# Optimization experiments

Measured on AMD Instinct MI355X. Metric: run time of the kernel, lower is better.

The kernel has to match this reference:

```python
import jax, jax.numpy as jnp
import numpy as np

B, N, U = 8, 4096, 128
AVG_DEG = 32.0  # expected neighbors per node


def setup_inputs() -> dict:
    key = jax.random.key(0)
    k1, k2, k3 = jax.random.split(key, 3)
    x = jax.random.normal(k1, (B, N, U), dtype=jnp.float32)
    # sparse-ish binary adjacency, ~AVG_DEG neighbors per node
    adj = (jax.random.uniform(k2, (B, N, N)) < (AVG_DEG / N)).astype(jnp.float32)
    W = jax.random.normal(k3, (U, U), dtype=jnp.float32) * 0.05
    b = jnp.zeros((U,), dtype=jnp.float32)
    return {"x": x, "adj": adj, "W": W, "b": b}


def reference(x, adj, W, b):
    # adjacency is stop_gradient'd in the original module
    adj = jax.lax.stop_gradient(adj)

    def step(h):
        # batched SpMM (dense here): [B,N,N] @ [B,N,U] -> [B,N,U]
        hn = jnp.einsum('bij,bjd->bid', adj, h)
        # aggregate_mode='graph_conv': no degree normalization
        return jax.nn.swish(hn @ W + b)

    # eval mode: K_l = 2 message-passing iterations
    return step(step(x))
```

## Files before the change

### kernel.cpp

```cpp
#include <hip/hip_runtime.h>
#include <math.h>

#define BB 8
#define NN 4096
#define UU 128
#define CAP 128
#define RPB 8

typedef float f4_t __attribute__((ext_vector_type(4)));

__device__ __forceinline__ void gather_gemm_swish(
    const unsigned short* __restrict__ sidx,
    const int* __restrict__ sdeg,
    float (*shn)[UU],
    const float* __restrict__ hsrc,
    const float* __restrict__ Wm,
    const float* __restrict__ bias,
    float* __restrict__ dst,
    int row0)
{
    const int rg   = threadIdx.x >> 5;
    const int lane = threadIdx.x & 31;
    const int row  = row0 + rg;
    const int b    = row >> 12;

    const float4* hb = (const float4*)(hsrc + (size_t)b * NN * UU);
    const unsigned short* my = &sidx[rg * CAP];
    const int d = sdeg[rg];

    float4 a0 = make_float4(0.f,0.f,0.f,0.f), a1 = a0, a2 = a0, a3 = a0;

    int n = 0;
    for (; n + 8 <= d; n += 8) {
        const int j0 = my[n+0], j1 = my[n+1], j2 = my[n+2], j3 = my[n+3];
        const int j4 = my[n+4], j5 = my[n+5], j6 = my[n+6], j7 = my[n+7];
        const float4 v0 = hb[j0 * 32 + lane];
        const float4 v1 = hb[j1 * 32 + lane];
        const float4 v2 = hb[j2 * 32 + lane];
        const float4 v3 = hb[j3 * 32 + lane];
        const float4 v4 = hb[j4 * 32 + lane];
        const float4 v5 = hb[j5 * 32 + lane];
        const float4 v6 = hb[j6 * 32 + lane];
        const float4 v7 = hb[j7 * 32 + lane];
        a0.x += v0.x + v4.x; a0.y += v0.y + v4.y; a0.z += v0.z + v4.z; a0.w += v0.w + v4.w;
        a1.x += v1.x + v5.x; a1.y += v1.y + v5.y; a1.z += v1.z + v5.z; a1.w += v1.w + v5.w;
        a2.x += v2.x + v6.x; a2.y += v2.y + v6.y; a2.z += v2.z + v6.z; a2.w += v2.w + v6.w;
        a3.x += v3.x + v7.x; a3.y += v3.y + v7.y; a3.z += v3.z + v7.z; a3.w += v3.w + v7.w;
    }
    if (n < d) {
        const int j0 = my[n+0], j1 = my[n+1], j2 = my[n+2], j3 = my[n+3];
        const int j4 = my[n+4], j5 = my[n+5], j6 = my[n+6], j7 = my[n+7];
        const float4 v0 = hb[j0 * 32 + lane];
        const float4 v1 = hb[j1 * 32 + lane];
        const float4 v2 = hb[j2 * 32 + lane];
        const float4 v3 = hb[j3 * 32 + lane];
        const float4 v4 = hb[j4 * 32 + lane];
        const float4 v5 = hb[j5 * 32 + lane];
        const float4 v6 = hb[j6 * 32 + lane];
        const float4 v7 = hb[j7 * 32 + lane];
        const float m0 = (n+0 < d) ? 1.f : 0.f, m1 = (n+1 < d) ? 1.f : 0.f;
        const float m2 = (n+2 < d) ? 1.f : 0.f, m3 = (n+3 < d) ? 1.f : 0.f;
        const float m4 = (n+4 < d) ? 1.f : 0.f, m5 = (n+5 < d) ? 1.f : 0.f;
        const float m6 = (n+6 < d) ? 1.f : 0.f, m7 = (n+7 < d) ? 1.f : 0.f;
        a0.x += v0.x*m0 + v4.x*m4; a0.y += v0.y*m0 + v4.y*m4; a0.z += v0.z*m0 + v4.z*m4; a0.w += v0.w*m0 + v4.w*m4;
        a1.x += v1.x*m1 + v5.x*m5; a1.y += v1.y*m1 + v5.y*m5; a1.z += v1.z*m1 + v5.z*m5; a1.w += v1.w*m1 + v5.w*m5;
        a2.x += v2.x*m2 + v6.x*m6; a2.y += v2.y*m2 + v6.y*m6; a2.z += v2.z*m2 + v6.z*m6; a2.w += v2.w*m2 + v6.w*m6;
        a3.x += v3.x*m3 + v7.x*m7; a3.y += v3.y*m3 + v7.y*m7; a3.z += v3.z*m3 + v7.z*m7; a3.w += v3.w*m3 + v7.w*m7;
    }

    float4 acc;
    acc.x = (a0.x + a1.x) + (a2.x + a3.x);
    acc.y = (a0.y + a1.y) + (a2.y + a3.y);
    acc.z = (a0.z + a1.z) + (a2.z + a3.z);
    acc.w = (a0.w + a1.w) + (a2.w + a3.w);
    ((float4*)shn[rg])[lane] = acc;
    __syncthreads();

    float ac0 = 0.f, ac1 = 0.f, ac2 = 0.f, ac3 = 0.f;
    const float4* W4 = (const float4*)Wm;
    const float* hr = shn[rg];
    #pragma unroll 4
    for (int k = 0; k < UU; k += 4) {
        const float4 w0 = W4[(k + 0) * 32 + lane];
        const float4 w1 = W4[(k + 1) * 32 + lane];
        const float4 w2 = W4[(k + 2) * 32 + lane];
        const float4 w3 = W4[(k + 3) * 32 + lane];
        const float4 sv = *(const float4*)&hr[k];
        ac0 += sv.x * w0.x + sv.y * w1.x + sv.z * w2.x + sv.w * w3.x;
        ac1 += sv.x * w0.y + sv.y * w1.y + sv.z * w2.y + sv.w * w3.y;
        ac2 += sv.x * w0.z + sv.y * w1.z + sv.z * w2.z + sv.w * w3.z;
        ac3 += sv.x * w0.w + sv.y * w1.w + sv.z * w2.w + sv.w * w3.w;
    }
    const float4 bb4 = ((const float4*)bias)[lane];
    float4 o; float v;
    v = ac0 + bb4.x; o.x = v / (1.f + expf(-v));
    v = ac1 + bb4.y; o.y = v / (1.f + expf(-v));
    v = ac2 + bb4.z; o.z = v / (1.f + expf(-v));
    v = ac3 + bb4.w; o.w = v / (1.f + expf(-v));
    ((float4*)dst)[(size_t)row * 32 + lane] = o;
}

__global__ __launch_bounds__(256) void hop1_kernel(
    const float* __restrict__ x,
    const float* __restrict__ adj,
    const float* __restrict__ Wm,
    const float* __restrict__ bias,
    unsigned short* __restrict__ idx,
    int* __restrict__ deg,
    float* __restrict__ h1)
{
    __shared__ unsigned short sidx[RPB * CAP];
    __shared__ int scnt[RPB];
    __shared__ float shn[RPB][UU];

    const int row0 = blockIdx.x * RPB;
    if (threadIdx.x < RPB) scnt[threadIdx.x] = 0;
    __syncthreads();

    const f4_t* ab = (const f4_t*)(adj + (size_t)row0 * NN);
    #pragma unroll 8
    for (int i = 0; i < 32; ++i) {
        const int g  = i * 256 + (int)threadIdx.x;
        const f4_t a = __builtin_nontemporal_load(ab + g);
        const int rr = g >> 10;
        const int jb = (g & 1023) * 4;
        if (a[0] != 0.f) { int p = atomicAdd(&scnt[rr], 1); if (p < CAP) sidx[rr*CAP + p] = (unsigned short)(jb + 0); }
        if (a[1] != 0.f) { int p = atomicAdd(&scnt[rr], 1); if (p < CAP) sidx[rr*CAP + p] = (unsigned short)(jb + 1); }
        if (a[2] != 0.f) { int p = atomicAdd(&scnt[rr], 1); if (p < CAP) sidx[rr*CAP + p] = (unsigned short)(jb + 2); }
        if (a[3] != 0.f) { int p = atomicAdd(&scnt[rr], 1); if (p < CAP) sidx[rr*CAP + p] = (unsigned short)(jb + 3); }
    }
    __syncthreads();

    const int rg   = threadIdx.x >> 5;
    const int lane = threadIdx.x & 31;
    const int row  = row0 + rg;
    int d = scnt[rg]; if (d > CAP) d = CAP;
    const int dpad = (d + 7) & ~7;
    for (int t = d + lane; t < dpad; t += 32) sidx[rg*CAP + t] = 0;
    if (lane == 0) { scnt[rg] = d; deg[row] = d; }
    for (int t = lane; t < dpad; t += 32)
        idx[(size_t)row * CAP + t] = sidx[rg*CAP + t];
    __syncthreads();

    gather_gemm_swish(sidx, scnt, shn, x, Wm, bias, h1, row0);
}

__global__ __launch_bounds__(256) void hop2_kernel(
    const float* __restrict__ h1,
    const unsigned short* __restrict__ idx,
    const int* __restrict__ deg,
    const float* __restrict__ Wm,
    const float* __restrict__ bias,
    float* __restrict__ out)
{
    __shared__ unsigned short sidx[RPB * CAP];
    __shared__ int sdeg[RPB];
    __shared__ float shn[RPB][UU];

    const int row0 = blockIdx.x * RPB;
    const uint4* g = (const uint4*)(idx + (size_t)row0 * CAP);
    if (threadIdx.x < 128) ((uint4*)sidx)[threadIdx.x] = g[threadIdx.x];
    if (threadIdx.x < RPB) sdeg[threadIdx.x] = deg[row0 + threadIdx.x];
    __syncthreads();

    gather_gemm_swish(sidx, sdeg, shn, h1, Wm, bias, out, row0);
}

extern "C" void kernel_launch(void* const* d_in, const int* in_sizes, int n_in,
                              void* d_out, int out_size, void* d_ws, size_t ws_size,
                              hipStream_t stream)
{
    const float* x    = (const float*)d_in[0];
    const float* adj  = (const float*)d_in[1];
    const float* Wm   = (const float*)d_in[2];
    const float* bias = (const float*)d_in[3];
    float* out = (float*)d_out;

    const int R = BB * NN;

    char* ws = (char*)d_ws;
    unsigned short* idx = (unsigned short*)ws;
    int* deg = (int*)(ws + (size_t)R * CAP * sizeof(unsigned short));
    float* h1 = (float*)(ws + (size_t)R * CAP * sizeof(unsigned short)
                             + (size_t)R * sizeof(int));

    hop1_kernel<<<R / RPB, 256, 0, stream>>>(x, adj, Wm, bias, idx, deg, h1);
    hop2_kernel<<<R / RPB, 256, 0, stream>>>(h1, idx, deg, Wm, bias, out);
}
```

Baseline: 825.6 us.

## Split adjacency compaction into its own kernel and swizzle blocks across XCDs

Adjacency scanning moves out of the fused hop-1 kernel into a dedicated one-row-per-block index-building kernel. Both hops then run the same gather+GEMM kernel. Block IDs are remapped so consecutive rows land on the same XCD, which is meant to improve L2 locality of the gathered features within a batch. This adds a third launch and writes then rereads the indices, in exchange for a streaming scan with more parallelism and better cache reuse in the gathers.

After: 829.4 us. Within noise of the previous version (+0.5%).

```diff
diff --git a/kernel.cpp b/kernel.cpp
--- a/kernel.cpp
+++ b/kernel.cpp
@@ -6,8 +6,45 @@
 #define UU 128
 #define CAP 128
 #define RPB 8
+#define NXCD 8
 
 typedef float f4_t __attribute__((ext_vector_type(4)));
+
+__global__ __launch_bounds__(256) void build_idx_kernel(
+    const float* __restrict__ adj,
+    unsigned short* __restrict__ idx,
+    int* __restrict__ deg)
+{
+    const int bid = blockIdx.x;
+    const int row = (bid & (NXCD - 1)) * (BB * NN / NXCD) + (bid >> 3);
+
+    const f4_t* arow = (const f4_t*)(adj + (size_t)row * NN);
+
+    __shared__ int cnt;
+    __shared__ unsigned short sidx[CAP];
+    if (threadIdx.x == 0) cnt = 0;
+    __syncthreads();
+
+    #pragma unroll
+    for (int it = 0; it < 4; ++it) {
+        const int v = it * 256 + threadIdx.x;
+        const f4_t a = __builtin_nontemporal_load(arow + v);
+        const int jb = v * 4;
+        if (a[0] != 0.f) { int p = atomicAdd(&cnt, 1); if (p < CAP) sidx[p] = (unsigned short)(jb + 0); }
+        if (a[1] != 0.f) { int p = atomicAdd(&cnt, 1); if (p < CAP) sidx[p] = (unsigned short)(jb + 1); }
+        if (a[2] != 0.f) { int p = atomicAdd(&cnt, 1); if (p < CAP) sidx[p] = (unsigned short)(jb + 2); }
+        if (a[3] != 0.f) { int p = atomicAdd(&cnt, 1); if (p < CAP) sidx[p] = (unsigned short)(jb + 3); }
+    }
+    __syncthreads();
+
+    int d = cnt; if (d > CAP) d = CAP;
+    const int dpad = (d + 7) & ~7;
+    for (int t = d + (int)threadIdx.x; t < dpad; t += 256) sidx[t] = 0;
+    if (threadIdx.x == 0) deg[row] = d;
+    __syncthreads();
+    for (int t = (int)threadIdx.x; t < dpad; t += 256)
+        idx[(size_t)row * CAP + t] = sidx[t];
+}
 
 __device__ __forceinline__ void gather_gemm_swish(
     const unsigned short* __restrict__ sidx,
@@ -100,70 +137,28 @@
     ((float4*)dst)[(size_t)row * 32 + lane] = o;
 }
 
-__global__ __launch_bounds__(256) void hop1_kernel(
-    const float* __restrict__ x,
-    const float* __restrict__ adj,
-    const float* __restrict__ Wm,
-    const float* __restrict__ bias,
-    unsigned short* __restrict__ idx,
-    int* __restrict__ deg,
-    float* __restrict__ h1)
-{
-    __shared__ unsigned short sidx[RPB * CAP];
-    __shared__ int scnt[RPB];
-    __shared__ float shn[RPB][UU];
-
-    const int row0 = blockIdx.x * RPB;
-    if (threadIdx.x < RPB) scnt[threadIdx.x] = 0;
-    __syncthreads();
-
-    const f4_t* ab = (const f4_t*)(adj + (size_t)row0 * NN);
-    #pragma unroll 8
-    for (int i = 0; i < 32; ++i) {
-        const int g  = i * 256 + (int)threadIdx.x;
-        const f4_t a = __builtin_nontemporal_load(ab + g);
-        const int rr = g >> 10;
-        const int jb = (g & 1023) * 4;
-        if (a[0] != 0.f) { int p = atomicAdd(&scnt[rr], 1); if (p < CAP) sidx[rr*CAP + p] = (unsigned short)(jb + 0); }
-        if (a[1] != 0.f) { int p = atomicAdd(&scnt[rr], 1); if (p < CAP) sidx[rr*CAP + p] = (unsigned short)(jb + 1); }
-        if (a[2] != 0.f) { int p = atomicAdd(&scnt[rr], 1); if (p < CAP) sidx[rr*CAP + p] = (unsigned short)(jb + 2); }
-        if (a[3] != 0.f) { int p = atomicAdd(&scnt[rr], 1); if (p < CAP) sidx[rr*CAP + p] = (unsigned short)(jb + 3); }
-    }
-    __syncthreads();
-
-    const int rg   = threadIdx.x >> 5;
-    const int lane = threadIdx.x & 31;
-    const int row  = row0 + rg;
-    int d = scnt[rg]; if (d > CAP) d = CAP;
-    const int dpad = (d + 7) & ~7;
-    for (int t = d + lane; t < dpad; t += 32) sidx[rg*CAP + t] = 0;
-    if (lane == 0) { scnt[rg] = d; deg[row] = d; }
-    for (int t = lane; t < dpad; t += 32)
-        idx[(size_t)row * CAP + t] = sidx[rg*CAP + t];
-    __syncthreads();
-
-    gather_gemm_swish(sidx, scnt, shn, x, Wm, bias, h1, row0);
-}
-
-__global__ __launch_bounds__(256) void hop2_kernel(
-    const float* __restrict__ h1,
+__global__ __launch_bounds__(256) void agg_gemm_kernel(
+    const float* __restrict__ hsrc,
     const unsigned short* __restrict__ idx,
     const int* __restrict__ deg,
     const float* __restrict__ Wm,
     const float* __restrict__ bias,
-    float* __restrict__ out)
+    float* __restrict__ dst)
 {
     __shared__ unsigned short sidx[RPB * CAP];
     __shared__ int sdeg[RPB];
     __shared__ float shn[RPB][UU];
 
-    const int row0 = blockIdx.x * RPB;
+    const int bid = blockIdx.x;
+    const int rb  = (bid & (NXCD - 1)) * (BB * NN / RPB / NXCD) + (bid >> 3);
+    const int row0 = rb * RPB;
+
     const uint4* g = (const uint4*)(idx + (size_t)row0 * CAP);
     if (threadIdx.x < 128) ((uint4*)sidx)[threadIdx.x] = g[threadIdx.x];
     if (threadIdx.x < RPB) sdeg[threadIdx.x] = deg[row0 + threadIdx.x];
     __syncthreads();
 
-    gather_gemm_swish(sidx, sdeg, shn, h1, Wm, bias, out, row0);
+    gather_gemm_swish(sidx, sdeg, shn, hsrc, Wm, bias, dst, row0);
 }
 
 extern "C" void kernel_launch(void* const* d_in, const int* in_sizes, int n_in,
@@ -184,6 +179,9 @@
     float* h1 = (float*)(ws + (size_t)R * CAP * sizeof(unsigned short)
                              + (size_t)R * sizeof(int));
 
-    hop1_kernel<<<R / RPB, 256, 0, stream>>>(x, adj, Wm, bias, idx, deg, h1);
-    hop2_kernel<<<R / RPB, 256, 0, stream>>>(h1, idx, deg, Wm, bias, out);
+    build_idx_kernel<<<R, 256, 0, stream>>>(adj, idx, deg);
+
+    agg_gemm_kernel<<<R / RPB, 256, 0, stream>>>(x, idx, deg, Wm, bias, h1);
+
+    agg_gemm_kernel<<<R / RPB, 256, 0, stream>>>(h1, idx, deg, Wm, bias, out);
 }
```
